# Kernel optimization log

Hardware: AMD Instinct MI355X
Metric: run time of the kernel (lower is better)

## Reference

```python
import jax, jax.numpy as jnp
import numpy as np

B, N, C = 4, 2048, 1024
H = 16
HD = C // H
SCALE = HD ** -0.5


def setup_inputs() -> dict:
    key = jax.random.key(0)
    k1, k2, k3, k4 = jax.random.split(key, 4)
    x = jax.random.normal(k1, (B, N, C), dtype=jnp.float32)
    w_qkv = jax.random.normal(k2, (3 * C, C), dtype=jnp.float32) * (C ** -0.5)
    w_proj = jax.random.normal(k3, (C, C), dtype=jnp.float32) * (C ** -0.5)
    b_proj = jax.random.normal(k4, (C,), dtype=jnp.float32) * 0.01
    return {"x": x, "w_qkv": w_qkv, "w_proj": w_proj, "b_proj": b_proj}


def reference(x, w_qkv, w_proj, b_proj):
    qkv = jnp.einsum('bnc,dc->bnd', x, w_qkv)
    qkv = qkv.reshape(B, N, 3, H, HD).transpose(2, 0, 3, 1, 4)
    q, k, v = qkv[0], qkv[1], qkv[2]
    # scaled dot-product attention with explicit softmax (dropout p=0 -> identity)
    attn = jnp.einsum('bhqd,bhkd->bhqk', q, k) * SCALE
    attn = jax.nn.softmax(attn, axis=-1)
    out = jnp.einsum('bhqk,bhkd->bhqd', attn, v)
    out = out.transpose(0, 2, 1, 3).reshape(B, N, C)
    # output projection
    return jnp.einsum('bnc,dc->bnd', out, w_proj) + b_proj
```

## Files before the change

kernel.cpp:

```cpp
#include <hip/hip_runtime.h>

typedef unsigned short u16;
typedef unsigned int u32;
typedef __bf16 bf16x8 __attribute__((ext_vector_type(8)));
typedef __bf16 bf16x4 __attribute__((ext_vector_type(4)));
typedef short s16x4 __attribute__((ext_vector_type(4)));
typedef float f32x4 __attribute__((ext_vector_type(4)));
typedef float f32x16 __attribute__((ext_vector_type(16)));
typedef unsigned int u32x2 __attribute__((ext_vector_type(2)));
typedef unsigned int u32x4 __attribute__((ext_vector_type(4)));

struct __align__(8) u16x4 { u16 x, y, z, w; };

__device__ __forceinline__ void async_copy16(const void* g, void* l) {
  __builtin_amdgcn_global_load_lds(
      (__attribute__((address_space(1))) void*)g,
      (__attribute__((address_space(3))) void*)l, 16, 0, 0);
}

__device__ __forceinline__ u16 f2bf(float f) {
  unsigned u = __builtin_bit_cast(unsigned, f);
  u = (u + 0x7FFFu + ((u >> 16) & 1u)) >> 16;
  return (u16)u;
}
__device__ __forceinline__ float bf2f(u16 h) {
  unsigned u = ((unsigned)h) << 16;
  return __builtin_bit_cast(float, u);
}

__device__ __forceinline__ float fast_exp2(float x) {
  return __builtin_amdgcn_exp2f(x);
}
__device__ __forceinline__ float fast_rcp(float x) {
  return __builtin_amdgcn_rcpf(x);
}

__device__ __forceinline__ f32x4 mfma32(bf16x8 a, bf16x8 b, f32x4 c) {
  return __builtin_amdgcn_mfma_f32_16x16x32_bf16(a, b, c, 0, 0, 0);
}

__device__ __forceinline__ u32 cvt_pk_bf16(float lo, float hi) {
  u32 r;
  asm("v_cvt_pk_bf16_f32 %0, %1, %2" : "=v"(r) : "v"(lo), "v"(hi));
  return r;
}

#define CEXP 0.18033688011112042f

__global__ void detect_mode(const u32* __restrict__ probe, int* __restrict__ flag) {
  __shared__ int cnt[256];
  int t = threadIdx.x;
  int c = 0;
#pragma unroll
  for (int j = 0; j < 16; ++j) {
    u32 v = probe[t + j * 256];
    unsigned e = (v >> 7) & 0xFFu;
    c += (e >= 100u && e <= 130u) ? 1 : 0;
  }
  cnt[t] = c;
  __syncthreads();
  for (int s = 128; s > 0; s >>= 1) {
    if (t < s) cnt[t] += cnt[t + s];
    __syncthreads();
  }
  if (t == 0) *flag = (cnt[0] * 2 > 4096) ? 1 : 0;
}

__global__ void convert_in(const void* __restrict__ src, u16* __restrict__ dst,
                           const int* __restrict__ flag, int n) {
  int mode = *flag;
  int i = (blockIdx.x * blockDim.x + threadIdx.x) * 8;
  if (i >= n) return;
  if (mode == 1) {
    *(uint4*)(dst + i) = *(const uint4*)((const u16*)src + i);
  } else {
    const float* s = (const float*)src;
    float4 a = *(const float4*)(s + i);
    float4 b = *(const float4*)(s + i + 4);
    uint4 o;
    o.x = (u32)f2bf(a.x) | ((u32)f2bf(a.y) << 16);
    o.y = (u32)f2bf(a.z) | ((u32)f2bf(a.w) << 16);
    o.z = (u32)f2bf(b.x) | ((u32)f2bf(b.y) << 16);
    o.w = (u32)f2bf(b.z) | ((u32)f2bf(b.w) << 16);
    *(uint4*)(dst + i) = o;
  }
}

template<int NJ>
__global__ __launch_bounds__(512, 2) void gemm_bt(
    const u16* __restrict__ A, const u16* __restrict__ Bm,
    u16* __restrict__ C, u16* __restrict__ vT, const u16* __restrict__ bias,
    float* __restrict__ outF, const int* __restrict__ flagp,
    int K, int ldc)
{
  __shared__ __align__(16) char lds[65536 + NJ * 16384];

  const int t = threadIdx.x;
  const int lane = t & 63, wave = t >> 6;
  const int quad = lane >> 4, l16 = lane & 15;
  const int wn = wave & 3, wm = wave >> 2;

  const int nwg = gridDim.x * gridDim.y;
  int bid = blockIdx.y * gridDim.x + blockIdx.x;
  bid = (bid & 7) * (nwg >> 3) + (bid >> 3);
  const int rowbase = (bid / gridDim.x) * 256;
  const int colbase = (bid % gridDim.x) * (NJ * 64);

  const int srow = t >> 3;
  const int scol = ((t & 7) << 4) ^ ((srow & 7) << 4);
  const int wlds = wave << 10;

  const u16* Arow = A + (size_t)(rowbase + srow) * K + (scol >> 1);
  const u16* Brow = Bm + (size_t)(colbase + srow) * K + (scol >> 1);

  auto stageA = [&](int kb_, int buf_) {
#pragma unroll
    for (int q = 0; q < 4; ++q)
      async_copy16(Arow + (size_t)kb_ * 64 + (size_t)q * 64 * K,
                   lds + buf_ * 32768 + q * 8192 + wlds);
  };
  auto stageB = [&](int kb_, int buf_) {
#pragma unroll
    for (int q = 0; q < NJ; ++q)
      async_copy16(Brow + (size_t)kb_ * 64 + (size_t)q * 64 * K,
                   lds + 65536 + buf_ * (NJ * 8192) + q * 8192 + wlds);
  };

  f32x4 acc[8][NJ] = {};

  const int swzl = (l16 & 7) << 4;
  const int c0 = (quad * 16) ^ swzl;
  const int c1 = (64 + quad * 16) ^ swzl;
  const char* Ard = lds + (size_t)(wm * 128 + l16) * 128;
  const char* Brd = lds + 65536 + (size_t)(wn * (NJ * 16) + l16) * 128;

  stageA(0, 0); stageB(0, 0);
  stageA(1, 1); stageB(1, 1);
  if constexpr (NJ == 3) asm volatile("s_waitcnt vmcnt(7)" ::: "memory");
  else                   asm volatile("s_waitcnt vmcnt(6)" ::: "memory");
  __builtin_amdgcn_s_barrier();

  const int nkb = K >> 6;
  for (int kb = 0; kb < nkb; ++kb) {
    const int cur = kb & 1;
    const char* Ab = Ard + cur * 32768;
    const char* Bb = Brd + cur * (NJ * 8192);
    bf16x8 aR[4], bR[NJ][2];

#pragma unroll
    for (int i = 0; i < 4; ++i) aR[i] = *(const bf16x8*)(Ab + i * 2048 + c0);
#pragma unroll
    for (int j = 0; j < NJ; ++j) {
      bR[j][0] = *(const bf16x8*)(Bb + j * 2048 + c0);
      bR[j][1] = *(const bf16x8*)(Bb + j * 2048 + c1);
    }
    __builtin_amdgcn_s_barrier();
    __builtin_amdgcn_s_setprio(1);
#pragma unroll
    for (int i = 0; i < 4; ++i)
#pragma unroll
      for (int j = 0; j < NJ; ++j)
        acc[i][j] = mfma32(aR[i], bR[j][0], acc[i][j]);
    __builtin_amdgcn_s_setprio(0);
    __builtin_amdgcn_s_barrier();

#pragma unroll
    for (int i = 0; i < 4; ++i) aR[i] = *(const bf16x8*)(Ab + i * 2048 + c1);
    __builtin_amdgcn_s_barrier();
    __builtin_amdgcn_s_setprio(1);
#pragma unroll
    for (int i = 0; i < 4; ++i)
#pragma unroll
      for (int j = 0; j < NJ; ++j)
        acc[i][j] = mfma32(aR[i], bR[j][1], acc[i][j]);
    __builtin_amdgcn_s_setprio(0);
    __builtin_amdgcn_s_barrier();
    if (kb + 2 < nkb) stageB(kb + 2, cur);

#pragma unroll
    for (int i = 0; i < 4; ++i) aR[i] = *(const bf16x8*)(Ab + 8192 + i * 2048 + c1);
    __builtin_amdgcn_s_barrier();
    __builtin_amdgcn_s_setprio(1);
#pragma unroll
    for (int i = 0; i < 4; ++i)
#pragma unroll
      for (int j = 0; j < NJ; ++j)
        acc[4 + i][j] = mfma32(aR[i], bR[j][1], acc[4 + i][j]);
    __builtin_amdgcn_s_setprio(0);
    __builtin_amdgcn_s_barrier();

#pragma unroll
    for (int i = 0; i < 4; ++i) aR[i] = *(const bf16x8*)(Ab + 8192 + i * 2048 + c0);
    __builtin_amdgcn_s_barrier();
    __builtin_amdgcn_s_setprio(1);
#pragma unroll
    for (int i = 0; i < 4; ++i)
#pragma unroll
      for (int j = 0; j < NJ; ++j)
        acc[4 + i][j] = mfma32(aR[i], bR[j][0], acc[4 + i][j]);
    __builtin_amdgcn_s_setprio(0);
    __builtin_amdgcn_s_barrier();

    if (kb + 2 < nkb) {
      stageA(kb + 2, cur);
      if constexpr (NJ == 3) asm volatile("s_waitcnt vmcnt(7)" ::: "memory");
      else                   asm volatile("s_waitcnt vmcnt(6)" ::: "memory");
      __builtin_amdgcn_s_barrier();
    } else if (kb + 1 < nkb) {
      asm volatile("s_waitcnt vmcnt(0)" ::: "memory");
      __builtin_amdgcn_s_barrier();
    }
  }

  const bool f32out = (flagp != nullptr) && (*flagp == 0);
#pragma unroll
  for (int nj = 0; nj < NJ; ++nj) {
    int cg = colbase + wn * (NJ * 16) + nj * 16 + l16;
    if (vT != nullptr && cg >= 2048) {
#pragma unroll
      for (int mi = 0; mi < 8; ++mi) {
        int rg = rowbase + wm * 128 + mi * 16 + quad * 4;
        int b = rg >> 11, n = rg & 2047;
        size_t idx = ((size_t)(b * 1024 + (cg - 2048))) * 2048 + n;
        u16x4 pk;
        pk.x = f2bf(acc[mi][nj][0]); pk.y = f2bf(acc[mi][nj][1]);
        pk.z = f2bf(acc[mi][nj][2]); pk.w = f2bf(acc[mi][nj][3]);
        *(u16x4*)(vT + idx) = pk;
      }
    } else {
      const float scl = (vT != nullptr && cg < 1024) ? CEXP : 1.0f;
      float bv = bias ? bf2f(bias[cg]) : 0.0f;
#pragma unroll
      for (int mi = 0; mi < 8; ++mi) {
#pragma unroll
        for (int r = 0; r < 4; ++r) {
          int rg = rowbase + wm * 128 + mi * 16 + quad * 4 + r;
          float val = acc[mi][nj][r] * scl + bv;
          if (f32out) outF[(size_t)rg * ldc + cg] = val;
          else        C[(size_t)rg * ldc + cg] = f2bf(val);
        }
      }
    }
  }
}

__global__ __launch_bounds__(256, 4) void attn_fwd(
    const u16* __restrict__ qk, const u16* __restrict__ vT, u16* __restrict__ outp)
{
  __shared__ __align__(16) char sm[32768];

  const int t = threadIdx.x;
  const int lane = t & 63, wave = t >> 6;
  const int l31 = lane & 31, h32 = lane >> 5;
  const int bh = blockIdx.x, b = bh >> 4, h = bh & 15;
  const int qtile = blockIdx.y;
  const size_t row0 = (size_t)b * 2048;
  const int qb = qtile * 128 + wave * 32;

  bf16x8 qf[4];
  {
    const u16* qp = qk + (row0 + qb + l31) * 2048 + h * 64 + h32 * 8;
#pragma unroll
    for (int s = 0; s < 4; ++s)
      qf[s] = *(const bf16x8*)(qp + s * 16);
  }

  const u16* Kg[2]; const u16* Vg[2]; unsigned loff[2];
#pragma unroll
  for (int q = 0; q < 2; ++q) {
    int si = q * 256 + t;
    int srow = si >> 3;
    int scolb = ((si & 7) << 4) ^ ((srow & 7) << 4);
    Kg[q] = qk + (row0 + srow) * 2048 + 1024 + h * 64 + (scolb >> 1);
    Vg[q] = vT + ((size_t)(b * 1024 + h * 64 + srow)) * 2048 + (scolb >> 1);
    loff[q] = q * 4096 + wave * 1024;
  }

#pragma unroll
  for (int q = 0; q < 2; ++q) {
    async_copy16(Kg[q], sm + loff[q]);
    async_copy16(Vg[q], sm + 16384 + loff[q]);
  }

  const int swz = (lane & 7) << 4;
  int cswz[4];
#pragma unroll
  for (int s = 0; s < 4; ++s) cswz[s] = (s * 32 + h32 * 16) ^ swz;
  const int rowb = l31 * 128;

  f32x16 o2[2] = {};
  float lsum = 0.0f;

  for (int kb = 0; kb < 32; ++kb) {
    const int cur = kb & 1, nxt = cur ^ 1;
    __syncthreads();
    if (kb < 31) {
#pragma unroll
      for (int q = 0; q < 2; ++q) {
        async_copy16(Kg[q] + (size_t)(kb + 1) * 64 * 2048, sm + nxt * 8192 + loff[q]);
        async_copy16(Vg[q] + (kb + 1) * 64, sm + 16384 + nxt * 8192 + loff[q]);
      }
    }
    const char* Kb = sm + cur * 8192;
    const char* Vb = sm + 16384 + cur * 8192;

#pragma unroll
    for (int kh = 0; kh < 2; ++kh) {
      f32x16 s2 = {};
      __builtin_amdgcn_s_setprio(1);
#pragma unroll
      for (int s = 0; s < 4; ++s) {
        bf16x8 kf = *(const bf16x8*)(Kb + kh * 4096 + rowb + cswz[s]);
        s2 = __builtin_amdgcn_mfma_f32_32x32x16_bf16(kf, qf[s], s2, 0, 0, 0);
      }
      __builtin_amdgcn_s_setprio(0);

      u32 u[8];
#pragma unroll
      for (int w = 0; w < 8; ++w) {
        float p0 = fast_exp2(s2[2 * w]);
        float p1 = fast_exp2(s2[2 * w + 1]);
        lsum += p0 + p1;
        u[w] = cvt_pk_bf16(p0, p1);
      }

      u32x2 r02 = __builtin_amdgcn_permlane32_swap(u[0], u[2], false, false);
      u32x2 r13 = __builtin_amdgcn_permlane32_swap(u[1], u[3], false, false);
      u32x2 r46 = __builtin_amdgcn_permlane32_swap(u[4], u[6], false, false);
      u32x2 r57 = __builtin_amdgcn_permlane32_swap(u[5], u[7], false, false);
      u32x4 fa0v; fa0v.x = r02.x; fa0v.y = r13.x; fa0v.z = r02.y; fa0v.w = r13.y;
      u32x4 fa1v; fa1v.x = r46.x; fa1v.y = r57.x; fa1v.z = r46.y; fa1v.w = r57.y;
      bf16x8 fa0 = __builtin_bit_cast(bf16x8, fa0v);
      bf16x8 fa1 = __builtin_bit_cast(bf16x8, fa1v);

      __builtin_amdgcn_s_setprio(1);
#pragma unroll
      for (int eb = 0; eb < 2; ++eb) {
        bf16x8 v0 = *(const bf16x8*)(Vb + eb * 4096 + rowb + cswz[kh * 2 + 0]);
        o2[eb] = __builtin_amdgcn_mfma_f32_32x32x16_bf16(fa0, v0, o2[eb], 0, 0, 0);
        bf16x8 v1 = *(const bf16x8*)(Vb + eb * 4096 + rowb + cswz[kh * 2 + 1]);
        o2[eb] = __builtin_amdgcn_mfma_f32_32x32x16_bf16(fa1, v1, o2[eb], 0, 0, 0);
      }
      __builtin_amdgcn_s_setprio(0);
    }
  }

  lsum += __shfl_xor(lsum, 32, 64);
  float inv = fast_rcp(lsum);

#pragma unroll
  for (int r = 0; r < 16; ++r) {
    int qr = (r & 3) + 8 * (r >> 2) + 4 * h32;
    float iv = __shfl(inv, qr, 64);
    size_t base = (row0 + qb + qr) * 1024 + h * 64 + l31;
    outp[base]      = f2bf(o2[0][r] * iv);
    outp[base + 32] = f2bf(o2[1][r] * iv);
  }
}

extern "C" void kernel_launch(void* const* d_in, const int* in_sizes, int n_in,
                              void* d_out, int out_size, void* d_ws, size_t ws_size,
                              hipStream_t stream) {
  (void)in_sizes; (void)n_in; (void)out_size; (void)ws_size;
  const void* x_in     = d_in[0];
  const void* wqkv_in  = d_in[1];
  const void* wproj_in = d_in[2];
  const void* bproj_in = d_in[3];

  u16* qkbuf  = (u16*)d_ws;
  u16* vT     = qkbuf + 16777216;
  u16* xb     = vT + 8388608;
  u16* wqkvb  = xb + 8388608;
  int* flag   = (int*)(wqkvb + 3145728);
  u16* attn   = xb;
  u16* wprojb = vT;
  u16* bprojb = vT + 1048576;

  detect_mode<<<1, 256, 0, stream>>>((const u32*)wqkv_in, flag);
  convert_in<<<4096, 256, 0, stream>>>(x_in, xb, flag, 8388608);
  convert_in<<<1536, 256, 0, stream>>>(wqkv_in, wqkvb, flag, 3145728);

  gemm_bt<3><<<dim3(16, 32), 512, 0, stream>>>(xb, wqkvb, qkbuf, vT, nullptr,
                                               nullptr, nullptr, 1024, 2048);
  attn_fwd<<<dim3(64, 16), 256, 0, stream>>>(qkbuf, vT, attn);

  convert_in<<<512, 256, 0, stream>>>(wproj_in, wprojb, flag, 1048576);
  convert_in<<<1, 256, 0, stream>>>(bproj_in, bprojb, flag, 1024);

  gemm_bt<2><<<dim3(8, 32), 512, 0, stream>>>(attn, wprojb, (u16*)d_out, nullptr,
                                              bprojb, (float*)d_out, flag, 1024, 1024);
}
```

Baseline: 274.4 us.

## Merge GEMM k-phases for NJ=2, compute softmax row sums via MFMA, tighten attention waits

For the NJ=2 GEMM instantiation, both k-halves of A are loaded into registers at once, so each k-block runs two MFMA phases instead of four and needs fewer barriers. In the attention kernel, the row-sum of the bf16-rounded probabilities is now computed by extra MFMAs against a ones vector, replacing scalar FP32 adds and the final shuffles. Explicit vmcnt waits plus raw s_barrier replace __syncthreads so the next tile's async copies can stay in flight. This costs more registers in the GEMM and extra MFMA work in attention, and the normalizer now comes from bf16-rounded probabilities.

```diff
diff --git a/kernel.cpp b/kernel.cpp
--- a/kernel.cpp
+++ b/kernel.cpp
@@ -145,61 +145,105 @@
     const int cur = kb & 1;
     const char* Ab = Ard + cur * 32768;
     const char* Bb = Brd + cur * (NJ * 8192);
-    bf16x8 aR[4], bR[NJ][2];
-
-#pragma unroll
-    for (int i = 0; i < 4; ++i) aR[i] = *(const bf16x8*)(Ab + i * 2048 + c0);
-#pragma unroll
-    for (int j = 0; j < NJ; ++j) {
-      bR[j][0] = *(const bf16x8*)(Bb + j * 2048 + c0);
-      bR[j][1] = *(const bf16x8*)(Bb + j * 2048 + c1);
+
+    if constexpr (NJ == 2) {
+      bf16x8 aR[4][2], bR[2][2];
+#pragma unroll
+      for (int i = 0; i < 4; ++i) {
+        aR[i][0] = *(const bf16x8*)(Ab + i * 2048 + c0);
+        aR[i][1] = *(const bf16x8*)(Ab + i * 2048 + c1);
+      }
+#pragma unroll
+      for (int j = 0; j < 2; ++j) {
+        bR[j][0] = *(const bf16x8*)(Bb + j * 2048 + c0);
+        bR[j][1] = *(const bf16x8*)(Bb + j * 2048 + c1);
+      }
+      __builtin_amdgcn_s_barrier();
+      __builtin_amdgcn_s_setprio(1);
+#pragma unroll
+      for (int i = 0; i < 4; ++i)
+#pragma unroll
+        for (int j = 0; j < 2; ++j) {
+          acc[i][j] = mfma32(aR[i][0], bR[j][0], acc[i][j]);
+          acc[i][j] = mfma32(aR[i][1], bR[j][1], acc[i][j]);
+        }
+      __builtin_amdgcn_s_setprio(0);
+      __builtin_amdgcn_s_barrier();
+      if (kb + 2 < nkb) stageB(kb + 2, cur);
+
+#pragma unroll
+      for (int i = 0; i < 4; ++i) {
+        aR[i][0] = *(const bf16x8*)(Ab + 8192 + i * 2048 + c0);
+        aR[i][1] = *(const bf16x8*)(Ab + 8192 + i * 2048 + c1);
+      }
+      __builtin_amdgcn_s_barrier();
+      __builtin_amdgcn_s_setprio(1);
+#pragma unroll
+      for (int i = 0; i < 4; ++i)
+#pragma unroll
+        for (int j = 0; j < 2; ++j) {
+          acc[4 + i][j] = mfma32(aR[i][0], bR[j][0], acc[4 + i][j]);
+          acc[4 + i][j] = mfma32(aR[i][1], bR[j][1], acc[4 + i][j]);
+        }
+      __builtin_amdgcn_s_setprio(0);
+      __builtin_amdgcn_s_barrier();
+    } else {
+      bf16x8 aR[4], bR[NJ][2];
+
+#pragma unroll
+      for (int i = 0; i < 4; ++i) aR[i] = *(const bf16x8*)(Ab + i * 2048 + c0);
+#pragma unroll
+      for (int j = 0; j < NJ; ++j) {
+        bR[j][0] = *(const bf16x8*)(Bb + j * 2048 + c0);
+        bR[j][1] = *(const bf16x8*)(Bb + j * 2048 + c1);
+      }
+      __builtin_amdgcn_s_barrier();
+      __builtin_amdgcn_s_setprio(1);
+#pragma unroll
+      for (int i = 0; i < 4; ++i)
+#pragma unroll
+        for (int j = 0; j < NJ; ++j)
+          acc[i][j] = mfma32(aR[i], bR[j][0], acc[i][j]);
+      __builtin_amdgcn_s_setprio(0);
+      __builtin_amdgcn_s_barrier();
+
+#pragma unroll
+      for (int i = 0; i < 4; ++i) aR[i] = *(const bf16x8*)(Ab + i * 2048 + c1);
+      __builtin_amdgcn_s_barrier();
+      __builtin_amdgcn_s_setprio(1);
+#pragma unroll
+      for (int i = 0; i < 4; ++i)
+#pragma unroll
+        for (int j = 0; j < NJ; ++j)
+          acc[i][j] = mfma32(aR[i], bR[j][1], acc[i][j]);
+      __builtin_amdgcn_s_setprio(0);
+      __builtin_amdgcn_s_barrier();
+      if (kb + 2 < nkb) stageB(kb + 2, cur);
+
+#pragma unroll
+      for (int i = 0; i < 4; ++i) aR[i] = *(const bf16x8*)(Ab + 8192 + i * 2048 + c1);
+      __builtin_amdgcn_s_barrier();
+      __builtin_amdgcn_s_setprio(1);
+#pragma unroll
+      for (int i = 0; i < 4; ++i)
+#pragma unroll
+        for (int j = 0; j < NJ; ++j)
+          acc[4 + i][j] = mfma32(aR[i], bR[j][1], acc[4 + i][j]);
+      __builtin_amdgcn_s_setprio(0);
+      __builtin_amdgcn_s_barrier();
+
+#pragma unroll
+      for (int i = 0; i < 4; ++i) aR[i] = *(const bf16x8*)(Ab + 8192 + i * 2048 + c0);
+      __builtin_amdgcn_s_barrier();
+      __builtin_amdgcn_s_setprio(1);
+#pragma unroll
+      for (int i = 0; i < 4; ++i)
+#pragma unroll
+        for (int j = 0; j < NJ; ++j)
+          acc[4 + i][j] = mfma32(aR[i], bR[j][0], acc[4 + i][j]);
+      __builtin_amdgcn_s_setprio(0);
+      __builtin_amdgcn_s_barrier();
     }
-    __builtin_amdgcn_s_barrier();
-    __builtin_amdgcn_s_setprio(1);
-#pragma unroll
-    for (int i = 0; i < 4; ++i)
-#pragma unroll
-      for (int j = 0; j < NJ; ++j)
-        acc[i][j] = mfma32(aR[i], bR[j][0], acc[i][j]);
-    __builtin_amdgcn_s_setprio(0);
-    __builtin_amdgcn_s_barrier();
-
-#pragma unroll
-    for (int i = 0; i < 4; ++i) aR[i] = *(const bf16x8*)(Ab + i * 2048 + c1);
-    __builtin_amdgcn_s_barrier();
-    __builtin_amdgcn_s_setprio(1);
-#pragma unroll
-    for (int i = 0; i < 4; ++i)
-#pragma unroll
-      for (int j = 0; j < NJ; ++j)
-        acc[i][j] = mfma32(aR[i], bR[j][1], acc[i][j]);
-    __builtin_amdgcn_s_setprio(0);
-    __builtin_amdgcn_s_barrier();
-    if (kb + 2 < nkb) stageB(kb + 2, cur);
-
-#pragma unroll
-    for (int i = 0; i < 4; ++i) aR[i] = *(const bf16x8*)(Ab + 8192 + i * 2048 + c1);
-    __builtin_amdgcn_s_barrier();
-    __builtin_amdgcn_s_setprio(1);
-#pragma unroll
-    for (int i = 0; i < 4; ++i)
-#pragma unroll
-      for (int j = 0; j < NJ; ++j)
-        acc[4 + i][j] = mfma32(aR[i], bR[j][1], acc[4 + i][j]);
-    __builtin_amdgcn_s_setprio(0);
-    __builtin_amdgcn_s_barrier();
-
-#pragma unroll
-    for (int i = 0; i < 4; ++i) aR[i] = *(const bf16x8*)(Ab + 8192 + i * 2048 + c0);
-    __builtin_amdgcn_s_barrier();
-    __builtin_amdgcn_s_setprio(1);
-#pragma unroll
-    for (int i = 0; i < 4; ++i)
-#pragma unroll
-      for (int j = 0; j < NJ; ++j)
-        acc[4 + i][j] = mfma32(aR[i], bR[j][0], acc[4 + i][j]);
-    __builtin_amdgcn_s_setprio(0);
-    __builtin_amdgcn_s_barrier();
 
     if (kb + 2 < nkb) {
       stageA(kb + 2, cur);
@@ -288,19 +332,28 @@
   for (int s = 0; s < 4; ++s) cswz[s] = (s * 32 + h32 * 16) ^ swz;
   const int rowb = l31 * 128;
 
+  u32x4 onev; onev.x = 0x3F803F80u; onev.y = 0x3F803F80u;
+  onev.z = 0x3F803F80u; onev.w = 0x3F803F80u;
+  const bf16x8 ones = __builtin_bit_cast(bf16x8, onev);
+
   f32x16 o2[2] = {};
-  float lsum = 0.0f;
+  f32x16 o3 = {};
 
   for (int kb = 0; kb < 32; ++kb) {
     const int cur = kb & 1, nxt = cur ^ 1;
-    __syncthreads();
+    __builtin_amdgcn_s_barrier();
     if (kb < 31) {
 #pragma unroll
       for (int q = 0; q < 2; ++q) {
         async_copy16(Kg[q] + (size_t)(kb + 1) * 64 * 2048, sm + nxt * 8192 + loff[q]);
         async_copy16(Vg[q] + (kb + 1) * 64, sm + 16384 + nxt * 8192 + loff[q]);
       }
+      asm volatile("s_waitcnt vmcnt(4)" ::: "memory");
+    } else {
+      asm volatile("s_waitcnt vmcnt(0)" ::: "memory");
     }
+    __builtin_amdgcn_s_barrier();
+
     const char* Kb = sm + cur * 8192;
     const char* Vb = sm + 16384 + cur * 8192;
 
@@ -320,7 +373,6 @@
       for (int w = 0; w < 8; ++w) {
         float p0 = fast_exp2(s2[2 * w]);
         float p1 = fast_exp2(s2[2 * w + 1]);
-        lsum += p0 + p1;
         u[w] = cvt_pk_bf16(p0, p1);
       }
 
@@ -341,17 +393,16 @@
         bf16x8 v1 = *(const bf16x8*)(Vb + eb * 4096 + rowb + cswz[kh * 2 + 1]);
         o2[eb] = __builtin_amdgcn_mfma_f32_32x32x16_bf16(fa1, v1, o2[eb], 0, 0, 0);
       }
+      o3 = __builtin_amdgcn_mfma_f32_32x32x16_bf16(fa0, ones, o3, 0, 0, 0);
+      o3 = __builtin_amdgcn_mfma_f32_32x32x16_bf16(fa1, ones, o3, 0, 0, 0);
       __builtin_amdgcn_s_setprio(0);
     }
   }
-
-  lsum += __shfl_xor(lsum, 32, 64);
-  float inv = fast_rcp(lsum);
 
 #pragma unroll
   for (int r = 0; r < 16; ++r) {
     int qr = (r & 3) + 8 * (r >> 2) + 4 * h32;
-    float iv = __shfl(inv, qr, 64);
+    float iv = fast_rcp(o3[r]);
     size_t base = (row0 + qb + qr) * 1024 + h * 64 + l31;
     outp[base]      = f2bf(o2[0][r] * iv);
     outp[base + 32] = f2bf(o2[1][r] * iv);
```

Result: no change. 275.2 us (+0.3%).
